# Performance work log

Hardware: AMD Instinct MI355X
Metric: run time of the kernel (lower is better)

The kernel has to match this reference:

```python
import jax, jax.numpy as jnp
import numpy as np

N = 32767      # 2**15 - 1 nodes: complete binary tree, parent(i) = (i-1)//2
IN = 512       # in_channels
H = 256        # hidden_dim
OUT = 1        # output_dim
DEPTH = 15     # number of topological levels (static)


def setup_inputs() -> dict:
    key = jax.random.key(0)
    ks = jax.random.split(key, 8)
    x = jax.random.normal(ks[0], (N, IN), dtype=jnp.float32)
    # complete binary tree edge list: edge_index[0]=child, edge_index[1]=parent
    src = jnp.arange(1, N, dtype=jnp.int32)
    dst = (src - 1) // 2
    edge_index = jnp.stack([src, dst])  # [2, N-1]
    s = 1.0 / np.sqrt(H)  # torch LSTMCell/Linear default uniform init scale
    W_ih = jax.random.uniform(ks[1], (4 * H, IN), minval=-s, maxval=s, dtype=jnp.float32)
    W_hh = jax.random.uniform(ks[2], (4 * H, H), minval=-s, maxval=s, dtype=jnp.float32)
    b_ih = jax.random.uniform(ks[3], (4 * H,), minval=-s, maxval=s, dtype=jnp.float32)
    b_hh = jax.random.uniform(ks[4], (4 * H,), minval=-s, maxval=s, dtype=jnp.float32)
    W_fc = jax.random.uniform(ks[5], (OUT, H), minval=-s, maxval=s, dtype=jnp.float32)
    b_fc = jax.random.uniform(ks[6], (OUT,), minval=-s, maxval=s, dtype=jnp.float32)
    return {"x": x, "edge_index": edge_index, "W_ih": W_ih, "W_hh": W_hh,
            "b_ih": b_ih, "b_hh": b_hh, "W_fc": W_fc, "b_fc": b_fc}


def reference(x, edge_index, W_ih, W_hh, b_ih, b_hh, W_fc, b_fc):
    src, dst = edge_index[0], edge_index[1]
    # children count per parent (matches torch children_count loop)
    cnt = jax.ops.segment_sum(jnp.ones_like(src, dtype=x.dtype), dst, num_segments=N)
    cnt = jnp.maximum(cnt, 1.0)[:, None]  # [N,1]; leaves get zero child state anyway
    h = jnp.zeros((N, H), dtype=x.dtype)
    c = jnp.zeros((N, H), dtype=x.dtype)
    # topological sweep: deepest level first (children processed before parents)
    for d in range(DEPTH - 1, -1, -1):
        lo = 2 ** d - 1
        hi = min(2 ** (d + 1) - 1, N)  # level d node index range (static)
        # mean of already-computed child h/c states, gathered via edge list
        mean_h = jax.ops.segment_sum(h[src], dst, num_segments=N)[lo:hi] / cnt[lo:hi]
        mean_c = jax.ops.segment_sum(c[src], dst, num_segments=N)[lo:hi] / cnt[lo:hi]
        # torch LSTMCell: gates in (i, f, g, o) order
        gates = x[lo:hi] @ W_ih.T + b_ih + mean_h @ W_hh.T + b_hh  # [n_level, 4H]
        i, f, g, o = jnp.split(gates, 4, axis=-1)
        i, f, o = jax.nn.sigmoid(i), jax.nn.sigmoid(f), jax.nn.sigmoid(o)
        g = jnp.tanh(g)
        c_new = f * mean_c + i * g
        h_new = o * jnp.tanh(c_new)
        h = h.at[lo:hi].set(h_new)
        c = c.at[lo:hi].set(c_new)
    pooled = jnp.mean(h, axis=0, keepdims=True)  # [1, H]
    out = pooled @ W_fc.T + b_fc                 # [1, 1]
    return out.squeeze(-1)                       # [1]
```

## Files before the change

### kernel.cpp

```cpp
#include <hip/hip_runtime.h>
#include <math.h>


#define N_NODES 32767
#define N_LEAF0 16383
#define IN_C    512
#define H_C     256

typedef __bf16 bf16x8 __attribute__((ext_vector_type(8)));
typedef float  f32x4  __attribute__((ext_vector_type(4)));

__device__ __forceinline__ void gload_lds16(const void* g, void* l) {
    __builtin_amdgcn_global_load_lds(
        (const __attribute__((address_space(1))) unsigned int*)g,
        (__attribute__((address_space(3))) unsigned int*)l,
        16, 0, 0);
}

__device__ __forceinline__ float fast_rcp(float x) { return __builtin_amdgcn_rcpf(x); }
__device__ __forceinline__ float sigm(float x)     { return fast_rcp(1.f + __expf(-x)); }
__device__ __forceinline__ float tanh_fast(float x){ return 2.f * fast_rcp(1.f + __expf(-2.f * x)) - 1.f; }

__global__ __launch_bounds__(256)
void conv_bf16_kernel(const float* __restrict__ src, __bf16* __restrict__ dst, int n8)
{
    const int i = blockIdx.x * 256 + threadIdx.x;
    if (i < n8) {
        const float4* s4 = (const float4*)src;
        const float4 a = s4[2 * i];
        const float4 b = s4[2 * i + 1];
        bf16x8 o;
        o[0] = (__bf16)a.x; o[1] = (__bf16)a.y; o[2] = (__bf16)a.z; o[3] = (__bf16)a.w;
        o[4] = (__bf16)b.x; o[5] = (__bf16)b.y; o[6] = (__bf16)b.z; o[7] = (__bf16)b.w;
        *(bf16x8*)(dst + 8 * i) = o;
    }
}

__global__ __launch_bounds__(256)
void bulk_xw(const float* __restrict__ x,
             const __bf16* __restrict__ wih,
             const float* __restrict__ b_ih,
             const float* __restrict__ b_hh,
             __bf16* __restrict__ hb,
             float* __restrict__ c,
             __bf16* __restrict__ gx)
{
    __shared__ __bf16 As[128 * 32];
    __shared__ __bf16 Bs[128 * 32];

    const int t    = threadIdx.x;
    const int lane = t & 63;
    const int wv   = t >> 6;
    const int wm   = wv >> 1;
    const int wn   = wv & 1;
    const int quad = lane >> 4;
    const int l15  = lane & 15;
    const int cb   = blockIdx.x;
    const int m0   = blockIdx.y * 128;

    f32x4 acc[4][4];
#pragma unroll
    for (int mi = 0; mi < 4; ++mi)
#pragma unroll
        for (int ni = 0; ni < 4; ++ni) acc[mi][ni] = (f32x4)0.f;

    for (int k0 = 0; k0 < IN_C; k0 += 32) {
#pragma unroll
        for (int e = 0; e < 2; ++e) {
            const int chunk = wv * 2 + e;
            const int nl    = chunk * 16 + (lane >> 2);
            const int q     = (nl >> 4) & 3;
            const int cc    = (nl & 15) + ((nl >> 6) << 4);
            const int grow  = q * H_C + cb * 32 + cc;
            const void* g = (const char*)(wih + grow * IN_C + k0) + (lane & 3) * 16;
            gload_lds16(g, (char*)Bs + chunk * 1024);
        }
        {
            const int row  = t >> 1;
            const int kh   = (t & 1) * 16;
            const int node = min(m0 + row, N_NODES - 1);
            const float4* xs = (const float4*)(x + (size_t)node * IN_C + k0 + kh);
            const float4 v0 = xs[0], v1 = xs[1], v2 = xs[2], v3 = xs[3];
            bf16x8 o0, o1;
            o0[0] = (__bf16)v0.x; o0[1] = (__bf16)v0.y; o0[2] = (__bf16)v0.z; o0[3] = (__bf16)v0.w;
            o0[4] = (__bf16)v1.x; o0[5] = (__bf16)v1.y; o0[6] = (__bf16)v1.z; o0[7] = (__bf16)v1.w;
            o1[0] = (__bf16)v2.x; o1[1] = (__bf16)v2.y; o1[2] = (__bf16)v2.z; o1[3] = (__bf16)v2.w;
            o1[4] = (__bf16)v3.x; o1[5] = (__bf16)v3.y; o1[6] = (__bf16)v3.z; o1[7] = (__bf16)v3.w;
            bf16x8* dst = (bf16x8*)(As + row * 32 + kh);
            dst[0] = o0;
            dst[1] = o1;
        }
        __syncthreads();
        bf16x8 af[4], bfr[4];
#pragma unroll
        for (int mi = 0; mi < 4; ++mi)
            af[mi] = *(const bf16x8*)(As + (wm * 64 + mi * 16 + l15) * 32 + quad * 8);
#pragma unroll
        for (int ni = 0; ni < 4; ++ni)
            bfr[ni] = *(const bf16x8*)(Bs + (wn * 64 + ni * 16 + l15) * 32 + quad * 8);
#pragma unroll
        for (int mi = 0; mi < 4; ++mi)
#pragma unroll
            for (int ni = 0; ni < 4; ++ni)
                acc[mi][ni] = __builtin_amdgcn_mfma_f32_16x16x32_bf16(
                    af[mi], bfr[ni], acc[mi][ni], 0, 0, 0);
        __syncthreads();
    }

    const int CH = cb * 32 + wn * 16 + l15;
    float bs[4];
#pragma unroll
    for (int q = 0; q < 4; ++q) bs[q] = b_ih[q * H_C + CH] + b_hh[q * H_C + CH];

#pragma unroll
    for (int mi = 0; mi < 4; ++mi) {
#pragma unroll
        for (int r = 0; r < 4; ++r) {
            const int m = m0 + wm * 64 + mi * 16 + quad * 4 + r;
            if (m >= N_NODES) continue;
            if (m >= N_LEAF0) {
                const float gi = sigm(acc[mi][0][r] + bs[0]);
                const float gf = sigm(acc[mi][1][r] + bs[1]);  (void)gf;
                const float gg = tanh_fast(acc[mi][2][r] + bs[2]);
                const float go = sigm(acc[mi][3][r] + bs[3]);
                const float cn = gi * gg;
                const float hn = go * tanh_fast(cn);
                c[(size_t)m * H_C + CH] = cn;
                hb[(size_t)m * H_C + CH] = (__bf16)hn;
            } else {
#pragma unroll
                for (int q = 0; q < 4; ++q)
                    gx[(size_t)m * 1024 + q * H_C + CH] = (__bf16)acc[mi][q][r];
            }
        }
    }
}

__global__ __launch_bounds__(256)
void level_hw(const __bf16* __restrict__ whh,
              const float* __restrict__ b_ih,
              const float* __restrict__ b_hh,
              const __bf16* __restrict__ gx,
              __bf16* __restrict__ hb,
              float* __restrict__ c,
              int lo, int n)
{
    __shared__ __bf16 As[128 * 32];
    __shared__ __bf16 Bs[128 * 32];

    const int t    = threadIdx.x;
    const int lane = t & 63;
    const int wv   = t >> 6;
    const int wm   = wv >> 1;
    const int wn   = wv & 1;
    const int quad = lane >> 4;
    const int l15  = lane & 15;
    const int cb   = blockIdx.x;
    const int m0   = blockIdx.y * 128;

    f32x4 acc[4][4];
#pragma unroll
    for (int mi = 0; mi < 4; ++mi)
#pragma unroll
        for (int ni = 0; ni < 4; ++ni) acc[mi][ni] = (f32x4)0.f;

    for (int k0 = 0; k0 < H_C; k0 += 32) {
#pragma unroll
        for (int e = 0; e < 2; ++e) {
            const int chunk = wv * 2 + e;
            const int nl    = chunk * 16 + (lane >> 2);
            const int q     = (nl >> 4) & 3;
            const int cc    = (nl & 15) + ((nl >> 6) << 4);
            const int grow  = q * H_C + cb * 32 + cc;
            const void* g = (const char*)(whh + grow * H_C + k0) + (lane & 3) * 16;
            gload_lds16(g, (char*)Bs + chunk * 1024);
        }
        {
            const int row  = t >> 1;
            const int kh   = (t & 1) * 16;
            const int node = lo + m0 + row;
            const int k2   = k0 + kh;
            const bf16x8* hl = (const bf16x8*)(hb + (size_t)(2 * node + 1) * H_C + k2);
            const bf16x8* hr = (const bf16x8*)(hb + (size_t)(2 * node + 2) * H_C + k2);
            const bf16x8 a0 = hl[0], a1 = hl[1], b0 = hr[0], b1 = hr[1];
            bf16x8 o0, o1;
#pragma unroll
            for (int j = 0; j < 8; ++j) {
                o0[j] = (__bf16)(0.5f * ((float)a0[j] + (float)b0[j]));
                o1[j] = (__bf16)(0.5f * ((float)a1[j] + (float)b1[j]));
            }
            bf16x8* dst = (bf16x8*)(As + row * 32 + kh);
            dst[0] = o0;
            dst[1] = o1;
        }
        __syncthreads();
        bf16x8 af[4], bfr[4];
#pragma unroll
        for (int mi = 0; mi < 4; ++mi)
            af[mi] = *(const bf16x8*)(As + (wm * 64 + mi * 16 + l15) * 32 + quad * 8);
#pragma unroll
        for (int ni = 0; ni < 4; ++ni)
            bfr[ni] = *(const bf16x8*)(Bs + (wn * 64 + ni * 16 + l15) * 32 + quad * 8);
#pragma unroll
        for (int mi = 0; mi < 4; ++mi)
#pragma unroll
            for (int ni = 0; ni < 4; ++ni)
                acc[mi][ni] = __builtin_amdgcn_mfma_f32_16x16x32_bf16(
                    af[mi], bfr[ni], acc[mi][ni], 0, 0, 0);
        __syncthreads();
    }

    const int CH = cb * 32 + wn * 16 + l15;
    float bs[4];
#pragma unroll
    for (int q = 0; q < 4; ++q) bs[q] = b_ih[q * H_C + CH] + b_hh[q * H_C + CH];

#pragma unroll
    for (int mi = 0; mi < 4; ++mi) {
#pragma unroll
        for (int r = 0; r < 4; ++r) {
            const int m = m0 + wm * 64 + mi * 16 + quad * 4 + r;
            if (m < n) {
                const int node = lo + m;
                const float g0 = acc[mi][0][r] + (float)gx[(size_t)node * 1024 + 0 * H_C + CH] + bs[0];
                const float g1 = acc[mi][1][r] + (float)gx[(size_t)node * 1024 + 1 * H_C + CH] + bs[1];
                const float g2 = acc[mi][2][r] + (float)gx[(size_t)node * 1024 + 2 * H_C + CH] + bs[2];
                const float g3 = acc[mi][3][r] + (float)gx[(size_t)node * 1024 + 3 * H_C + CH] + bs[3];
                const float gi = sigm(g0);
                const float gf = sigm(g1);
                const float gg = tanh_fast(g2);
                const float go = sigm(g3);
                const float mc = 0.5f * (c[(size_t)(2 * node + 1) * H_C + CH] +
                                         c[(size_t)(2 * node + 2) * H_C + CH]);
                const float cn = gf * mc + gi * gg;
                const float hn = go * tanh_fast(cn);
                c[(size_t)node * H_C + CH] = cn;
                hb[(size_t)node * H_C + CH] = (__bf16)hn;
            }
        }
    }
}

__global__ __launch_bounds__(256)
void reduce_rows(const __bf16* __restrict__ hb, float* __restrict__ part)
{
    const int tcol = threadIdx.x;
    const int b = blockIdx.x;
    float s = 0.f;
    for (int r = 0; r < 128; ++r) {
        const int row = b * 128 + r;
        if (row < N_NODES) s += (float)hb[(size_t)row * H_C + tcol];
    }
    part[b * H_C + tcol] = s;
}

__global__ __launch_bounds__(256)
void reduce_final(const float* __restrict__ part,
                  const float* __restrict__ W_fc,
                  const float* __restrict__ b_fc,
                  float* __restrict__ out)
{
    __shared__ float sm[256];
    const int t = threadIdx.x;
    float s = 0.f;
    for (int j = 0; j < 256; ++j) s += part[j * H_C + t];
    s = s * (1.0f / (float)N_NODES) * W_fc[t];
    sm[t] = s;
    __syncthreads();
    for (int st = 128; st > 0; st >>= 1) {
        if (t < st) sm[t] += sm[t + st];
        __syncthreads();
    }
    if (t == 0) out[0] = sm[0] + b_fc[0];
}

extern "C" void kernel_launch(void* const* d_in, const int* in_sizes, int n_in,
                              void* d_out, int out_size, void* d_ws, size_t ws_size,
                              hipStream_t stream)
{
    const float* x    = (const float*)d_in[0];
    const float* W_ih = (const float*)d_in[2];
    const float* W_hh = (const float*)d_in[3];
    const float* b_ih = (const float*)d_in[4];
    const float* b_hh = (const float*)d_in[5];
    const float* W_fc = (const float*)d_in[6];
    const float* b_fc = (const float*)d_in[7];
    float* out = (float*)d_out;

    char* w = (char*)d_ws;
    __bf16* hb   = (__bf16*)w;  w += (size_t)N_NODES * H_C * 2;
    float*  c    = (float*)w;   w += (size_t)N_NODES * H_C * 4;
    __bf16* gx   = (__bf16*)w;  w += (size_t)N_LEAF0 * 1024 * 2;
    __bf16* wihb = (__bf16*)w;  w += (size_t)4 * H_C * IN_C * 2;
    __bf16* whhb = (__bf16*)w;  w += (size_t)4 * H_C * H_C * 2;
    float*  part = (float*)w;

    {
        const int n8i = (4 * H_C * IN_C) / 8;
        conv_bf16_kernel<<<(n8i + 255) / 256, 256, 0, stream>>>(W_ih, wihb, n8i);
        const int n8h = (4 * H_C * H_C) / 8;
        conv_bf16_kernel<<<(n8h + 255) / 256, 256, 0, stream>>>(W_hh, whhb, n8h);
    }

    {
        dim3 grid(8, 256);
        bulk_xw<<<grid, 256, 0, stream>>>(x, wihb, b_ih, b_hh, hb, c, gx);
    }
    for (int d = 13; d >= 0; --d) {
        const int n  = 1 << d;
        const int lo = n - 1;
        dim3 grid(8, (n + 127) / 128);
        level_hw<<<grid, 256, 0, stream>>>(whhb, b_ih, b_hh, gx, hb, c, lo, n);
    }
    reduce_rows<<<256, 256, 0, stream>>>(hb, part);
    reduce_final<<<1, 256, 0, stream>>>(part, W_fc, b_fc, out);
}
```

Measured before the change: 449.2 us.

## Fuse per-level LSTM launches into one cooperative kernel with grid sync

```diff
diff --git a/kernel.cpp b/kernel.cpp
--- a/kernel.cpp
+++ b/kernel.cpp
@@ -1,5 +1,8 @@
 #include <hip/hip_runtime.h>
+#include <hip/hip_cooperative_groups.h>
 #include <math.h>
+
+namespace cg = cooperative_groups;
 
 
 #define N_NODES 32767
@@ -8,6 +11,7 @@
 #define H_C     256
 
 typedef __bf16 bf16x8 __attribute__((ext_vector_type(8)));
+typedef __bf16 bf16x4 __attribute__((ext_vector_type(4)));
 typedef float  f32x4  __attribute__((ext_vector_type(4)));
 
 __device__ __forceinline__ void gload_lds16(const void* g, void* l) {
@@ -55,8 +59,9 @@
     const int wn   = wv & 1;
     const int quad = lane >> 4;
     const int l15  = lane & 15;
-    const int cb   = blockIdx.x;
-    const int m0   = blockIdx.y * 128;
+    const int bx   = blockIdx.x;
+    const int cb   = bx >> 8;
+    const int m0   = (bx & 255) * 128;
 
     f32x4 acc[4][4];
 #pragma unroll
@@ -120,7 +125,6 @@
             if (m >= N_NODES) continue;
             if (m >= N_LEAF0) {
                 const float gi = sigm(acc[mi][0][r] + bs[0]);
-                const float gf = sigm(acc[mi][1][r] + bs[1]);  (void)gf;
                 const float gg = tanh_fast(acc[mi][2][r] + bs[2]);
                 const float go = sigm(acc[mi][3][r] + bs[3]);
                 const float cn = gi * gg;
@@ -128,25 +132,27 @@
                 c[(size_t)m * H_C + CH] = cn;
                 hb[(size_t)m * H_C + CH] = (__bf16)hn;
             } else {
-#pragma unroll
-                for (int q = 0; q < 4; ++q)
-                    gx[(size_t)m * 1024 + q * H_C + CH] = (__bf16)acc[mi][q][r];
+                bf16x4 g4;
+#pragma unroll
+                for (int q = 0; q < 4; ++q) g4[q] = (__bf16)acc[mi][q][r];
+                *(bf16x4*)(gx + (size_t)m * 1024 + CH * 4) = g4;
             }
         }
     }
 }
 
 __global__ __launch_bounds__(256)
-void level_hw(const __bf16* __restrict__ whh,
-              const float* __restrict__ b_ih,
-              const float* __restrict__ b_hh,
-              const __bf16* __restrict__ gx,
-              __bf16* __restrict__ hb,
-              float* __restrict__ c,
-              int lo, int n)
-{
+void levels_fused(const __bf16* __restrict__ whh,
+                  const float* __restrict__ b_ih,
+                  const float* __restrict__ b_hh,
+                  const __bf16* __restrict__ gx,
+                  __bf16* __restrict__ hb,
+                  float* __restrict__ c)
+{
+    cg::grid_group gg_ = cg::this_grid();
+
+    __shared__ __bf16 Bfull[8 * 128 * 32];
     __shared__ __bf16 As[128 * 32];
-    __shared__ __bf16 Bs[128 * 32];
 
     const int t    = threadIdx.x;
     const int lane = t & 63;
@@ -155,16 +161,13 @@
     const int wn   = wv & 1;
     const int quad = lane >> 4;
     const int l15  = lane & 15;
-    const int cb   = blockIdx.x;
-    const int m0   = blockIdx.y * 128;
-
-    f32x4 acc[4][4];
-#pragma unroll
-    for (int mi = 0; mi < 4; ++mi)
-#pragma unroll
-        for (int ni = 0; ni < 4; ++ni) acc[mi][ni] = (f32x4)0.f;
-
-    for (int k0 = 0; k0 < H_C; k0 += 32) {
+    const int bx   = blockIdx.x;
+
+    const int cb = bx & 7;
+    const int mt = bx >> 3;
+
+#pragma unroll
+    for (int kc = 0; kc < 8; ++kc) {
 #pragma unroll
         for (int e = 0; e < 2; ++e) {
             const int chunk = wv * 2 + e;
@@ -172,72 +175,92 @@
             const int q     = (nl >> 4) & 3;
             const int cc    = (nl & 15) + ((nl >> 6) << 4);
             const int grow  = q * H_C + cb * 32 + cc;
-            const void* g = (const char*)(whh + grow * H_C + k0) + (lane & 3) * 16;
-            gload_lds16(g, (char*)Bs + chunk * 1024);
-        }
-        {
-            const int row  = t >> 1;
-            const int kh   = (t & 1) * 16;
-            const int node = lo + m0 + row;
-            const int k2   = k0 + kh;
-            const bf16x8* hl = (const bf16x8*)(hb + (size_t)(2 * node + 1) * H_C + k2);
-            const bf16x8* hr = (const bf16x8*)(hb + (size_t)(2 * node + 2) * H_C + k2);
-            const bf16x8 a0 = hl[0], a1 = hl[1], b0 = hr[0], b1 = hr[1];
-            bf16x8 o0, o1;
-#pragma unroll
-            for (int j = 0; j < 8; ++j) {
-                o0[j] = (__bf16)(0.5f * ((float)a0[j] + (float)b0[j]));
-                o1[j] = (__bf16)(0.5f * ((float)a1[j] + (float)b1[j]));
+            const void* g = (const char*)(whh + grow * H_C + kc * 32) + (lane & 3) * 16;
+            gload_lds16(g, (char*)Bfull + kc * 8192 + chunk * 1024);
+        }
+    }
+    __syncthreads();
+
+    const int CH = cb * 32 + wn * 16 + l15;
+    const float bs0 = b_ih[0 * H_C + CH] + b_hh[0 * H_C + CH];
+    const float bs1 = b_ih[1 * H_C + CH] + b_hh[1 * H_C + CH];
+    const float bs2 = b_ih[2 * H_C + CH] + b_hh[2 * H_C + CH];
+    const float bs3 = b_ih[3 * H_C + CH] + b_hh[3 * H_C + CH];
+
+
+    for (int d = 13; d >= 0; --d) {
+        const int n  = 1 << d;
+        const int lo = n - 1;
+        const int nm = (d > 7) ? (1 << (d - 7)) : 1;
+        if (mt < nm) {
+            const int m0 = mt * 128;
+
+            f32x4 acc[4][4];
+#pragma unroll
+            for (int mi = 0; mi < 4; ++mi)
+#pragma unroll
+                for (int ni = 0; ni < 4; ++ni) acc[mi][ni] = (f32x4)0.f;
+
+            for (int kc = 0; kc < 8; ++kc) {
+                {
+                    const int row  = t >> 1;
+                    const int kh   = (t & 1) * 16;
+                    const int node = lo + m0 + row;
+                    const int k2   = kc * 32 + kh;
+                    const bf16x8* hl = (const bf16x8*)(hb + (size_t)(2 * node + 1) * H_C + k2);
+                    const bf16x8* hr = (const bf16x8*)(hb + (size_t)(2 * node + 2) * H_C + k2);
+                    const bf16x8 a0 = hl[0], a1 = hl[1], b0 = hr[0], b1 = hr[1];
+                    bf16x8 o0, o1;
+#pragma unroll
+                    for (int j = 0; j < 8; ++j) {
+                        o0[j] = (__bf16)(0.5f * ((float)a0[j] + (float)b0[j]));
+                        o1[j] = (__bf16)(0.5f * ((float)a1[j] + (float)b1[j]));
+                    }
+                    bf16x8* dst = (bf16x8*)(As + row * 32 + kh);
+                    dst[0] = o0;
+                    dst[1] = o1;
+                }
+                __syncthreads();
+                bf16x8 af[4], bfr[4];
+#pragma unroll
+                for (int mi = 0; mi < 4; ++mi)
+                    af[mi] = *(const bf16x8*)(As + (wm * 64 + mi * 16 + l15) * 32 + quad * 8);
+#pragma unroll
+                for (int ni = 0; ni < 4; ++ni)
+                    bfr[ni] = *(const bf16x8*)(Bfull + kc * 4096 +
+                                               (wn * 64 + ni * 16 + l15) * 32 + quad * 8);
+#pragma unroll
+                for (int mi = 0; mi < 4; ++mi)
+#pragma unroll
+                    for (int ni = 0; ni < 4; ++ni)
+                        acc[mi][ni] = __builtin_amdgcn_mfma_f32_16x16x32_bf16(
+                            af[mi], bfr[ni], acc[mi][ni], 0, 0, 0);
+                __syncthreads();
             }
-            bf16x8* dst = (bf16x8*)(As + row * 32 + kh);
-            dst[0] = o0;
-            dst[1] = o1;
-        }
-        __syncthreads();
-        bf16x8 af[4], bfr[4];
-#pragma unroll
-        for (int mi = 0; mi < 4; ++mi)
-            af[mi] = *(const bf16x8*)(As + (wm * 64 + mi * 16 + l15) * 32 + quad * 8);
-#pragma unroll
-        for (int ni = 0; ni < 4; ++ni)
-            bfr[ni] = *(const bf16x8*)(Bs + (wn * 64 + ni * 16 + l15) * 32 + quad * 8);
-#pragma unroll
-        for (int mi = 0; mi < 4; ++mi)
-#pragma unroll
-            for (int ni = 0; ni < 4; ++ni)
-                acc[mi][ni] = __builtin_amdgcn_mfma_f32_16x16x32_bf16(
-                    af[mi], bfr[ni], acc[mi][ni], 0, 0, 0);
-        __syncthreads();
-    }
-
-    const int CH = cb * 32 + wn * 16 + l15;
-    float bs[4];
-#pragma unroll
-    for (int q = 0; q < 4; ++q) bs[q] = b_ih[q * H_C + CH] + b_hh[q * H_C + CH];
-
-#pragma unroll
-    for (int mi = 0; mi < 4; ++mi) {
-#pragma unroll
-        for (int r = 0; r < 4; ++r) {
-            const int m = m0 + wm * 64 + mi * 16 + quad * 4 + r;
-            if (m < n) {
-                const int node = lo + m;
-                const float g0 = acc[mi][0][r] + (float)gx[(size_t)node * 1024 + 0 * H_C + CH] + bs[0];
-                const float g1 = acc[mi][1][r] + (float)gx[(size_t)node * 1024 + 1 * H_C + CH] + bs[1];
-                const float g2 = acc[mi][2][r] + (float)gx[(size_t)node * 1024 + 2 * H_C + CH] + bs[2];
-                const float g3 = acc[mi][3][r] + (float)gx[(size_t)node * 1024 + 3 * H_C + CH] + bs[3];
-                const float gi = sigm(g0);
-                const float gf = sigm(g1);
-                const float gg = tanh_fast(g2);
-                const float go = sigm(g3);
-                const float mc = 0.5f * (c[(size_t)(2 * node + 1) * H_C + CH] +
-                                         c[(size_t)(2 * node + 2) * H_C + CH]);
-                const float cn = gf * mc + gi * gg;
-                const float hn = go * tanh_fast(cn);
-                c[(size_t)node * H_C + CH] = cn;
-                hb[(size_t)node * H_C + CH] = (__bf16)hn;
+
+#pragma unroll
+            for (int mi = 0; mi < 4; ++mi) {
+#pragma unroll
+                for (int r = 0; r < 4; ++r) {
+                    const int m = m0 + wm * 64 + mi * 16 + quad * 4 + r;
+                    if (m < n) {
+                        const int node = lo + m;
+                        const bf16x4 g4 = *(const bf16x4*)(gx + (size_t)node * 1024 + CH * 4);
+                        const float gi = sigm(acc[mi][0][r] + (float)g4[0] + bs0);
+                        const float gf = sigm(acc[mi][1][r] + (float)g4[1] + bs1);
+                        const float gt = tanh_fast(acc[mi][2][r] + (float)g4[2] + bs2);
+                        const float go = sigm(acc[mi][3][r] + (float)g4[3] + bs3);
+                        const float mc = 0.5f * (c[(size_t)(2 * node + 1) * H_C + CH] +
+                                                 c[(size_t)(2 * node + 2) * H_C + CH]);
+                        const float cn = gf * mc + gi * gt;
+                        const float hn = go * tanh_fast(cn);
+                        c[(size_t)node * H_C + CH] = cn;
+                        hb[(size_t)node * H_C + CH] = (__bf16)hn;
+                    }
+                }
             }
         }
+        gg_.sync();
     }
 }
 
@@ -302,16 +325,15 @@
         conv_bf16_kernel<<<(n8h + 255) / 256, 256, 0, stream>>>(W_hh, whhb, n8h);
     }
 
+    bulk_xw<<<2048, 256, 0, stream>>>(x, wihb, b_ih, b_hh, hb, c, gx);
+
     {
-        dim3 grid(8, 256);
-        bulk_xw<<<grid, 256, 0, stream>>>(x, wihb, b_ih, b_hh, hb, c, gx);
-    }
-    for (int d = 13; d >= 0; --d) {
-        const int n  = 1 << d;
-        const int lo = n - 1;
-        dim3 grid(8, (n + 127) / 128);
-        level_hw<<<grid, 256, 0, stream>>>(whhb, b_ih, b_hh, gx, hb, c, lo, n);
-    }
+        void* args[] = { (void*)&whhb, (void*)&b_ih, (void*)&b_hh,
+                         (void*)&gx, (void*)&hb, (void*)&c };
+        hipLaunchCooperativeKernel((const void*)levels_fused,
+                                   dim3(512), dim3(256), args, 0, stream);
+    }
+
     reduce_rows<<<256, 256, 0, stream>>>(hb, part);
     reduce_final<<<1, 256, 0, stream>>>(part, W_fc, b_fc, out);
 }
```

After: 1.164 ms. 2.59x slower.
